# Kernel optimization log

Hardware: AMD Instinct MI355X
Metric: run time of the kernel (lower is better)

## Reference

```python
import jax, jax.numpy as jnp
import numpy as np

TOP_K = 2

def setup_inputs() -> dict:
    key = jax.random.key(0)
    k0, k1, k2, k3, k4 = jax.random.split(key, 5)
    B, S, D, H, E = 2, 2048, 1024, 2048, 8
    x = jax.random.normal(k0, (B, S, D), dtype=jnp.float32)
    router_w = jax.random.normal(k1, (D, E), dtype=jnp.float32) * (1.0 / np.sqrt(D))
    wg = jax.random.normal(k2, (E, D, H), dtype=jnp.float32) * (1.0 / np.sqrt(D))
    wu = jax.random.normal(k3, (E, D, H), dtype=jnp.float32) * (1.0 / np.sqrt(D))
    wd = jax.random.normal(k4, (E, H, D), dtype=jnp.float32) * (1.0 / np.sqrt(H))
    return {"x": x, "router_w": router_w, "wg": wg, "wu": wu, "wd": wd}

def reference(x, router_w, wg, wu, wd):
    B, S, D = x.shape
    E = router_w.shape[1]
    xf = x.reshape(-1, D)                                   # [T, D]
    router_logits = xf @ router_w                           # [T, E]
    top_logits, top_idx = jax.lax.top_k(router_logits, TOP_K)
    top_w = jax.nn.softmax(top_logits, axis=-1)             # [T, k]
    # Dense combine weights: W[t, e] = routing weight if e in top-k of t, else 0.
    combine = jnp.sum(jax.nn.one_hot(top_idx, E, dtype=x.dtype) * top_w[..., None], axis=1)  # [T, E]
    # SwiGLU experts, computed for all tokens and masked by the combine weights
    # (mathematically identical to the gather/scatter form in the original).
    gate = jnp.einsum('td,edh->eth', xf, wg)                # [E, T, H]
    up = jnp.einsum('td,edh->eth', xf, wu)                  # [E, T, H]
    fused = jax.nn.silu(gate) * up                          # [E, T, H]
    expert_out = jnp.einsum('eth,ehd->etd', fused, wd)      # [E, T, D]
    y = jnp.einsum('etd,te->td', expert_out, combine)       # [T, D]
    return y.reshape(B, S, D)
```

## Files before the change

kernel.cpp:

```cpp
#include <hip/hip_runtime.h>
#include <hip/hip_bf16.h>

#define T_TOK 4096
#define DDIM  1024
#define HDIM  2048
#define NEXP  8
#define MAXSLOT 9216

typedef __attribute__((ext_vector_type(4))) float f32x4;
typedef __attribute__((ext_vector_type(8))) short s16x8;
typedef __hip_bfloat16 bf16;

typedef const void __attribute__((address_space(1))) gvoid;
typedef void __attribute__((address_space(3))) svoid;

__device__ __forceinline__ void gload16(const void* g, void* l) {
    __builtin_amdgcn_global_load_lds((gvoid*)g, (svoid*)l, 16, 0, 0);
}

__device__ __forceinline__ int frag_off(int rr, int kq) {
    int lr = rr >> 1;
    int ch = ((rr & 1) << 2) + (kq >> 3);
    return lr * 64 + (ch ^ (lr & 7)) * 8;
}

__global__ void router_cast_kernel(const float* __restrict__ x, const float* __restrict__ rw,
                                   int* __restrict__ r_e, float* __restrict__ r_w,
                                   bf16* __restrict__ xb) {
    int wave = threadIdx.x >> 6, lane = threadIdx.x & 63;
    int t = blockIdx.x * 4 + wave;
    const float* xr = x + (size_t)t * DDIM;
    bf16* xbr = xb + (size_t)t * DDIM;
    double acc[NEXP];
#pragma unroll
    for (int e = 0; e < NEXP; ++e) acc[e] = 0.0;
#pragma unroll
    for (int c = 0; c < 4; ++c) {
        int d = c * 256 + lane * 4;
        float4 v = *reinterpret_cast<const float4*>(xr + d);
        union { ushort4 u; bf16 h[4]; } o;
        o.h[0] = __float2bfloat16(v.x);
        o.h[1] = __float2bfloat16(v.y);
        o.h[2] = __float2bfloat16(v.z);
        o.h[3] = __float2bfloat16(v.w);
        *reinterpret_cast<ushort4*>(xbr + d) = o.u;
        const float* rw0 = rw + (size_t)d * NEXP;
#pragma unroll
        for (int j = 0; j < 4; ++j) {
            float xv = (&v.x)[j];
            const float* rwr = rw0 + j * NEXP;
#pragma unroll
            for (int e = 0; e < NEXP; ++e) acc[e] += (double)xv * (double)rwr[e];
        }
    }
#pragma unroll
    for (int e = 0; e < NEXP; ++e) {
#pragma unroll
        for (int off = 32; off > 0; off >>= 1) acc[e] += __shfl_down(acc[e], off);
    }
    if (lane == 0) {
        int i0 = 0; double v0 = acc[0];
#pragma unroll
        for (int e = 1; e < NEXP; ++e) if (acc[e] > v0) { v0 = acc[e]; i0 = e; }
        int i1 = -1; double v1 = -1e300;
#pragma unroll
        for (int e = 0; e < NEXP; ++e) { if (e == i0) continue; if (acc[e] > v1) { v1 = acc[e]; i1 = e; } }
        float w0 = 1.0f / (1.0f + expf((float)(v1 - v0)));
        float w1 = 1.0f - w0;
        r_e[2*t]   = i0; r_e[2*t+1] = i1;
        r_w[2*t]   = w0; r_w[2*t+1] = w1;
    }
}

__global__ void binning_kernel(const int* __restrict__ r_e, const float* __restrict__ r_w,
                               int* __restrict__ offs, int* __restrict__ cnt,
                               int* __restrict__ list, float* __restrict__ slot_w) {
    __shared__ int scnt[NEXP], scur[NEXP], soff[NEXP + 1];
    int tid = threadIdx.x;
    if (tid < NEXP) { scnt[tid] = 0; scur[tid] = 0; }
    __syncthreads();
    for (int i = tid; i < 2 * T_TOK; i += 512) atomicAdd(&scnt[r_e[i]], 1);
    __syncthreads();
    if (tid == 0) {
        int s = 0;
        for (int e = 0; e < NEXP; ++e) { soff[e] = s; s += (scnt[e] + 127) & ~127; }
        soff[NEXP] = s;
    }
    __syncthreads();
    if (tid < NEXP + 1) offs[tid] = soff[tid];
    if (tid < NEXP) cnt[tid] = scnt[tid];
    for (int i = tid; i < 2 * T_TOK; i += 512) {
        int e = r_e[i];
        int pos = atomicAdd(&scur[e], 1);
        int slot = soff[e] + pos;
        list[slot] = i >> 1;
        slot_w[slot] = r_w[i];
    }
}

__global__ void transpose_cast_kernel(const float* __restrict__ in, bf16* __restrict__ out,
                                      int R, int C, int rmul, int roff, size_t outE) {
    __shared__ bf16 tile[64][68];
    const float* inp = in + (size_t)blockIdx.z * R * C;
    bf16* outp = out + (size_t)blockIdx.z * outE;
    int r0 = blockIdx.x * 64, c0 = blockIdx.y * 64;
    int tid = threadIdx.x;
#pragma unroll
    for (int i = 0; i < 4; ++i) {
        int idx = i * 256 + tid;
        int r = idx >> 4, c4 = (idx & 15) * 4;
        float4 v = *reinterpret_cast<const float4*>(inp + (size_t)(r0 + r) * C + c0 + c4);
        union { ushort4 u; bf16 h[4]; } o;
        o.h[0] = __float2bfloat16(v.x);
        o.h[1] = __float2bfloat16(v.y);
        o.h[2] = __float2bfloat16(v.z);
        o.h[3] = __float2bfloat16(v.w);
        *reinterpret_cast<ushort4*>(&tile[r][c4]) = o.u;
    }
    __syncthreads();
#pragma unroll
    for (int i = 0; i < 4; ++i) {
        int idx = i * 256 + tid;
        int c = idx >> 4, r4 = (idx & 15) * 4;
        union { ushort4 u; bf16 h[4]; } w;
        w.h[0] = tile[r4 + 0][c];
        w.h[1] = tile[r4 + 1][c];
        w.h[2] = tile[r4 + 2][c];
        w.h[3] = tile[r4 + 3][c];
        *reinterpret_cast<ushort4*>(outp + ((size_t)(c0 + c) * rmul + roff) * R + r0 + r4) = w.u;
    }
}

__device__ __forceinline__ int find_expert(const int* offs, int slot0) {
    int e = 0;
#pragma unroll
    for (int i = 0; i < NEXP - 1; ++i) e += (offs[e + 1] <= slot0) ? 1 : 0;
    return e;
}

__global__ __launch_bounds__(256, 2)
void gateup_kernel(const bf16* __restrict__ xb, const bf16* __restrict__ wguT,
                   const int* __restrict__ offs, const int* __restrict__ cnt,
                   const int* __restrict__ list, bf16* __restrict__ hbuf) {
    int slot0 = blockIdx.y * 128;
    if (slot0 >= offs[NEXP]) return;
    int e = find_expert(offs, slot0);
    int base = offs[e];
    int ne = cnt[e];
    int m0 = slot0 - base;
    int n0 = blockIdx.x * 128;

    __shared__ bf16 As[2][4096];
    __shared__ bf16 Bs[2][4096];

    int tid = threadIdx.x, lane = tid & 63, wid = tid >> 6;

    const bf16* bbase = wguT + (size_t)e * (2 * HDIM) * DDIM + (size_t)n0 * DDIM;

    const bf16* aS[2]; const bf16* bS[2];
    int sdst[2];
#pragma unroll
    for (int j = 0; j < 2; ++j) {
        int q = wid + j * 4;
        int lr = q * 8 + (lane >> 3);
        int ch = (lane & 7) ^ (lr & 7);
        int rr = 2 * lr + (ch >> 2);
        int koff = (ch & 3) * 8;
        int r = m0 + rr; if (r > ne - 1) r = ne - 1;
        aS[j] = xb + (size_t)list[base + r] * DDIM + koff;
        bS[j] = bbase + (size_t)rr * DDIM + koff;
        sdst[j] = q * 512;
    }

    int rl = lane & 15, kq = 8 * (lane >> 4);
    int wrow = (wid >> 1) * 64;
    int wcol = (wid & 1) * 64;
    int offA[4], offB[4];
#pragma unroll
    for (int mi = 0; mi < 4; ++mi) offA[mi] = frag_off(wrow + mi * 16 + rl, kq);
#pragma unroll
    for (int ni = 0; ni < 4; ++ni) offB[ni] = frag_off(wcol + ni * 16 + rl, kq);

    f32x4 zero4 = {0.f, 0.f, 0.f, 0.f};
    f32x4 acc[4][4];
#pragma unroll
    for (int mi = 0; mi < 4; ++mi)
#pragma unroll
        for (int ni = 0; ni < 4; ++ni) acc[mi][ni] = zero4;

    const int nk = DDIM / 32;

#define GU_STAGE(tt, buf)                                     \
    {                                                         \
        int k0 = (tt) * 32;                                   \
        gload16(aS[0] + k0, &As[buf][sdst[0]]);               \
        gload16(aS[1] + k0, &As[buf][sdst[1]]);               \
        gload16(bS[0] + k0, &Bs[buf][sdst[0]]);               \
        gload16(bS[1] + k0, &Bs[buf][sdst[1]]);               \
    }

    GU_STAGE(0, 0);
    asm volatile("s_waitcnt vmcnt(0)" ::: "memory");
    __builtin_amdgcn_s_barrier();

    int cur = 0;
    for (int t = 0; t < nk; ++t) {
        if (t + 1 < nk) GU_STAGE(t + 1, cur ^ 1);
        const bf16* Ab = As[cur];
        const bf16* Bb = Bs[cur];
        s16x8 a[4], b[4];
#pragma unroll
        for (int mi = 0; mi < 4; ++mi) a[mi] = *reinterpret_cast<const s16x8*>(Ab + offA[mi]);
#pragma unroll
        for (int ni = 0; ni < 4; ++ni) b[ni] = *reinterpret_cast<const s16x8*>(Bb + offB[ni]);
        __builtin_amdgcn_s_setprio(1);
#pragma unroll
        for (int mi = 0; mi < 4; ++mi)
#pragma unroll
            for (int ni = 0; ni < 4; ++ni)
                acc[mi][ni] = __builtin_amdgcn_mfma_f32_16x16x32_bf16(a[mi], b[ni], acc[mi][ni], 0, 0, 0);
        __builtin_amdgcn_s_setprio(0);
        __builtin_amdgcn_sched_barrier(0);
        if (t + 1 < nk) {
            asm volatile("s_waitcnt vmcnt(0)" ::: "memory");
            __builtin_amdgcn_s_barrier();
        }
        cur ^= 1;
    }
#undef GU_STAGE

    int rbase = (lane >> 4) * 4, cbase = lane & 15;
    bool evenlane = (lane & 1) == 0;
#pragma unroll
    for (int mi = 0; mi < 4; ++mi) {
#pragma unroll
        for (int ni = 0; ni < 4; ++ni) {
#pragma unroll
            for (int r = 0; r < 4; ++r) {
                float own = acc[mi][ni][r];
                float oth = __shfl_xor(own, 1);
                int row = m0 + wrow + mi * 16 + rbase + r;
                if (evenlane && row < ne) {
                    float g = own, u = oth;
                    float h = (g / (1.0f + expf(-g))) * u;
                    int hcol = (n0 + wcol + ni * 16 + cbase) >> 1;
                    hbuf[(size_t)(base + row) * HDIM + hcol] = __float2bfloat16(h);
                }
            }
        }
    }
}

__global__ __launch_bounds__(256, 2)
void down_kernel(const bf16* __restrict__ hbuf, const bf16* __restrict__ wdT,
                 const int* __restrict__ offs, const int* __restrict__ cnt,
                 const int* __restrict__ list, const float* __restrict__ slot_w,
                 float* __restrict__ y) {
    int slot0 = blockIdx.y * 128;
    if (slot0 >= offs[NEXP]) return;
    int e = find_expert(offs, slot0);
    int base = offs[e];
    int ne = cnt[e];
    int m0 = slot0 - base;
    int n0 = blockIdx.x * 128;

    __shared__ bf16 As[2][4096];
    __shared__ bf16 Bs[2][4096];

    int tid = threadIdx.x, lane = tid & 63, wid = tid >> 6;

    const bf16* bbase = wdT + (size_t)e * DDIM * HDIM + (size_t)n0 * HDIM;

    const bf16* aS[2]; const bf16* bS[2];
    int sdst[2];
#pragma unroll
    for (int j = 0; j < 2; ++j) {
        int q = wid + j * 4;
        int lr = q * 8 + (lane >> 3);
        int ch = (lane & 7) ^ (lr & 7);
        int rr = 2 * lr + (ch >> 2);
        int koff = (ch & 3) * 8;
        int r = m0 + rr; if (r > ne - 1) r = ne - 1;
        aS[j] = hbuf + (size_t)(base + r) * HDIM + koff;
        bS[j] = bbase + (size_t)rr * HDIM + koff;
        sdst[j] = q * 512;
    }

    int rl = lane & 15, kq = 8 * (lane >> 4);
    int wrow = (wid >> 1) * 64;
    int wcol = (wid & 1) * 64;
    int offA[4], offB[4];
#pragma unroll
    for (int mi = 0; mi < 4; ++mi) offA[mi] = frag_off(wrow + mi * 16 + rl, kq);
#pragma unroll
    for (int ni = 0; ni < 4; ++ni) offB[ni] = frag_off(wcol + ni * 16 + rl, kq);

    f32x4 zero4 = {0.f, 0.f, 0.f, 0.f};
    f32x4 acc[4][4];
#pragma unroll
    for (int mi = 0; mi < 4; ++mi)
#pragma unroll
        for (int ni = 0; ni < 4; ++ni) acc[mi][ni] = zero4;

    const int nk = HDIM / 32;

#define DN_STAGE(tt, buf)                                     \
    {                                                         \
        int k0 = (tt) * 32;                                   \
        gload16(aS[0] + k0, &As[buf][sdst[0]]);               \
        gload16(aS[1] + k0, &As[buf][sdst[1]]);               \
        gload16(bS[0] + k0, &Bs[buf][sdst[0]]);               \
        gload16(bS[1] + k0, &Bs[buf][sdst[1]]);               \
    }

    DN_STAGE(0, 0);
    asm volatile("s_waitcnt vmcnt(0)" ::: "memory");
    __builtin_amdgcn_s_barrier();

    int cur = 0;
    for (int t = 0; t < nk; ++t) {
        if (t + 1 < nk) DN_STAGE(t + 1, cur ^ 1);
        const bf16* Ab = As[cur];
        const bf16* Bb = Bs[cur];
        s16x8 a[4], b[4];
#pragma unroll
        for (int mi = 0; mi < 4; ++mi) a[mi] = *reinterpret_cast<const s16x8*>(Ab + offA[mi]);
#pragma unroll
        for (int ni = 0; ni < 4; ++ni) b[ni] = *reinterpret_cast<const s16x8*>(Bb + offB[ni]);
        __builtin_amdgcn_s_setprio(1);
#pragma unroll
        for (int mi = 0; mi < 4; ++mi)
#pragma unroll
            for (int ni = 0; ni < 4; ++ni)
                acc[mi][ni] = __builtin_amdgcn_mfma_f32_16x16x32_bf16(a[mi], b[ni], acc[mi][ni], 0, 0, 0);
        __builtin_amdgcn_s_setprio(0);
        __builtin_amdgcn_sched_barrier(0);
        if (t + 1 < nk) {
            asm volatile("s_waitcnt vmcnt(0)" ::: "memory");
            __builtin_amdgcn_s_barrier();
        }
        cur ^= 1;
    }
#undef DN_STAGE

    int rbase = (lane >> 4) * 4, cbase = lane & 15;
#pragma unroll
    for (int mi = 0; mi < 4; ++mi) {
#pragma unroll
        for (int r = 0; r < 4; ++r) {
            int row = m0 + wrow + mi * 16 + rbase + r;
            if (row < ne) {
                int slot = base + row;
                int tok = list[slot];
                float w = slot_w[slot];
                float* yrow = y + (size_t)tok * DDIM + n0 + wcol + cbase;
#pragma unroll
                for (int ni = 0; ni < 4; ++ni)
                    atomicAdd(yrow + ni * 16, w * acc[mi][ni][r]);
            }
        }
    }
}

extern "C" void kernel_launch(void* const* d_in, const int* in_sizes, int n_in,
                              void* d_out, int out_size, void* d_ws, size_t ws_size,
                              hipStream_t stream) {
    const float* x  = (const float*)d_in[0];
    const float* rw = (const float*)d_in[1];
    const float* wg = (const float*)d_in[2];
    const float* wu = (const float*)d_in[3];
    const float* wd = (const float*)d_in[4];
    float* y = (float*)d_out;

    char* ws = (char*)d_ws;
    int*   r_e    = (int*)  (ws + 0);
    float* r_w    = (float*)(ws + 32768);
    int*   offs   = (int*)  (ws + 65600);
    int*   cnt    = (int*)  (ws + 65544 + 96);
    int*   list   = (int*)  (ws + 65664 + 128);
    float* slot_w = (float*)(ws + 65664 + 128 + 4 * MAXSLOT);
    bf16*  xb     = (bf16*) (ws + 1048576ull);
    bf16*  wguT   = (bf16*) (ws + 16777216ull);
    bf16*  wdT    = (bf16*) (ws + 83886080ull);
    bf16*  hbuf   = (bf16*) (ws + 117440512ull);

    transpose_cast_kernel<<<dim3(DDIM / 64, HDIM / 64, NEXP), 256, 0, stream>>>(
        wg, wguT, DDIM, HDIM, 2, 0, (size_t)2 * HDIM * DDIM);
    transpose_cast_kernel<<<dim3(DDIM / 64, HDIM / 64, NEXP), 256, 0, stream>>>(
        wu, wguT, DDIM, HDIM, 2, 1, (size_t)2 * HDIM * DDIM);
    transpose_cast_kernel<<<dim3(HDIM / 64, DDIM / 64, NEXP), 256, 0, stream>>>(
        wd, wdT, HDIM, DDIM, 1, 0, (size_t)DDIM * HDIM);

    router_cast_kernel<<<dim3(T_TOK / 4), 256, 0, stream>>>(x, rw, r_e, r_w, xb);
    binning_kernel<<<dim3(1), 512, 0, stream>>>(r_e, r_w, offs, cnt, list, slot_w);

    hipMemsetAsync(d_out, 0, (size_t)out_size * sizeof(float), stream);

    gateup_kernel<<<dim3(2 * HDIM / 128, MAXSLOT / 128, 1), 256, 0, stream>>>(
        xb, wguT, offs, cnt, list, hbuf);
    down_kernel<<<dim3(DDIM / 128, MAXSLOT / 128, 1), 256, 0, stream>>>(
        hbuf, wdT, offs, cnt, list, slot_w, y);
}
```

Baseline: 289.0 us.

## Triple-buffer GEMM K-loop prefetch and merge gate/up weight transposes

```diff
diff --git a/kernel.cpp b/kernel.cpp
--- a/kernel.cpp
+++ b/kernel.cpp
@@ -98,18 +98,20 @@
     }
 }
 
-__global__ void transpose_cast_kernel(const float* __restrict__ in, bf16* __restrict__ out,
-                                      int R, int C, int rmul, int roff, size_t outE) {
+__global__ void transpose_gu_kernel(const float* __restrict__ wg, const float* __restrict__ wu,
+                                    bf16* __restrict__ wguT) {
     __shared__ bf16 tile[64][68];
-    const float* inp = in + (size_t)blockIdx.z * R * C;
-    bf16* outp = out + (size_t)blockIdx.z * outE;
+    int which = blockIdx.z >> 3;
+    int e = blockIdx.z & 7;
+    const float* inp = (which ? wu : wg) + (size_t)e * DDIM * HDIM;
+    bf16* outp = wguT + (size_t)e * 2 * HDIM * DDIM;
     int r0 = blockIdx.x * 64, c0 = blockIdx.y * 64;
     int tid = threadIdx.x;
 #pragma unroll
     for (int i = 0; i < 4; ++i) {
         int idx = i * 256 + tid;
         int r = idx >> 4, c4 = (idx & 15) * 4;
-        float4 v = *reinterpret_cast<const float4*>(inp + (size_t)(r0 + r) * C + c0 + c4);
+        float4 v = *reinterpret_cast<const float4*>(inp + (size_t)(r0 + r) * HDIM + c0 + c4);
         union { ushort4 u; bf16 h[4]; } o;
         o.h[0] = __float2bfloat16(v.x);
         o.h[1] = __float2bfloat16(v.y);
@@ -127,7 +129,39 @@
         w.h[1] = tile[r4 + 1][c];
         w.h[2] = tile[r4 + 2][c];
         w.h[3] = tile[r4 + 3][c];
-        *reinterpret_cast<ushort4*>(outp + ((size_t)(c0 + c) * rmul + roff) * R + r0 + r4) = w.u;
+        *reinterpret_cast<ushort4*>(outp + ((size_t)(c0 + c) * 2 + which) * DDIM + r0 + r4) = w.u;
+    }
+}
+
+__global__ void transpose_wd_kernel(const float* __restrict__ wd, bf16* __restrict__ wdT) {
+    __shared__ bf16 tile[64][68];
+    const float* inp = wd + (size_t)blockIdx.z * HDIM * DDIM;
+    bf16* outp = wdT + (size_t)blockIdx.z * DDIM * HDIM;
+    int r0 = blockIdx.x * 64, c0 = blockIdx.y * 64;
+    int tid = threadIdx.x;
+#pragma unroll
+    for (int i = 0; i < 4; ++i) {
+        int idx = i * 256 + tid;
+        int r = idx >> 4, c4 = (idx & 15) * 4;
+        float4 v = *reinterpret_cast<const float4*>(inp + (size_t)(r0 + r) * DDIM + c0 + c4);
+        union { ushort4 u; bf16 h[4]; } o;
+        o.h[0] = __float2bfloat16(v.x);
+        o.h[1] = __float2bfloat16(v.y);
+        o.h[2] = __float2bfloat16(v.z);
+        o.h[3] = __float2bfloat16(v.w);
+        *reinterpret_cast<ushort4*>(&tile[r][c4]) = o.u;
+    }
+    __syncthreads();
+#pragma unroll
+    for (int i = 0; i < 4; ++i) {
+        int idx = i * 256 + tid;
+        int c = idx >> 4, r4 = (idx & 15) * 4;
+        union { ushort4 u; bf16 h[4]; } w;
+        w.h[0] = tile[r4 + 0][c];
+        w.h[1] = tile[r4 + 1][c];
+        w.h[2] = tile[r4 + 2][c];
+        w.h[3] = tile[r4 + 3][c];
+        *reinterpret_cast<ushort4*>(outp + (size_t)(c0 + c) * HDIM + r0 + r4) = w.u;
     }
 }
 
@@ -150,8 +184,8 @@
     int m0 = slot0 - base;
     int n0 = blockIdx.x * 128;
 
-    __shared__ bf16 As[2][4096];
-    __shared__ bf16 Bs[2][4096];
+    __shared__ bf16 As[3][4096];
+    __shared__ bf16 Bs[3][4096];
 
     int tid = threadIdx.x, lane = tid & 63, wid = tid >> 6;
 
@@ -200,14 +234,16 @@
     }
 
     GU_STAGE(0, 0);
-    asm volatile("s_waitcnt vmcnt(0)" ::: "memory");
+    GU_STAGE(1, 1);
+    asm volatile("s_waitcnt vmcnt(4)" ::: "memory");
     __builtin_amdgcn_s_barrier();
 
-    int cur = 0;
+    int cb = 0;
     for (int t = 0; t < nk; ++t) {
-        if (t + 1 < nk) GU_STAGE(t + 1, cur ^ 1);
-        const bf16* Ab = As[cur];
-        const bf16* Bb = Bs[cur];
+        int sb = cb + 2; if (sb >= 3) sb -= 3;
+        if (t + 2 < nk) GU_STAGE(t + 2, sb);
+        const bf16* Ab = As[cb];
+        const bf16* Bb = Bs[cb];
         s16x8 a[4], b[4];
 #pragma unroll
         for (int mi = 0; mi < 4; ++mi) a[mi] = *reinterpret_cast<const s16x8*>(Ab + offA[mi]);
@@ -222,10 +258,11 @@
         __builtin_amdgcn_s_setprio(0);
         __builtin_amdgcn_sched_barrier(0);
         if (t + 1 < nk) {
-            asm volatile("s_waitcnt vmcnt(0)" ::: "memory");
+            if (t + 2 < nk) asm volatile("s_waitcnt vmcnt(4)" ::: "memory");
+            else            asm volatile("s_waitcnt vmcnt(0)" ::: "memory");
             __builtin_amdgcn_s_barrier();
         }
-        cur ^= 1;
+        cb = cb + 1; if (cb >= 3) cb -= 3;
     }
 #undef GU_STAGE
 
@@ -264,8 +301,8 @@
     int m0 = slot0 - base;
     int n0 = blockIdx.x * 128;
 
-    __shared__ bf16 As[2][4096];
-    __shared__ bf16 Bs[2][4096];
+    __shared__ bf16 As[3][4096];
+    __shared__ bf16 Bs[3][4096];
 
     int tid = threadIdx.x, lane = tid & 63, wid = tid >> 6;
 
@@ -314,14 +351,16 @@
     }
 
     DN_STAGE(0, 0);
-    asm volatile("s_waitcnt vmcnt(0)" ::: "memory");
+    DN_STAGE(1, 1);
+    asm volatile("s_waitcnt vmcnt(4)" ::: "memory");
     __builtin_amdgcn_s_barrier();
 
-    int cur = 0;
+    int cb = 0;
     for (int t = 0; t < nk; ++t) {
-        if (t + 1 < nk) DN_STAGE(t + 1, cur ^ 1);
-        const bf16* Ab = As[cur];
-        const bf16* Bb = Bs[cur];
+        int sb = cb + 2; if (sb >= 3) sb -= 3;
+        if (t + 2 < nk) DN_STAGE(t + 2, sb);
+        const bf16* Ab = As[cb];
+        const bf16* Bb = Bs[cb];
         s16x8 a[4], b[4];
 #pragma unroll
         for (int mi = 0; mi < 4; ++mi) a[mi] = *reinterpret_cast<const s16x8*>(Ab + offA[mi]);
@@ -336,10 +375,11 @@
         __builtin_amdgcn_s_setprio(0);
         __builtin_amdgcn_sched_barrier(0);
         if (t + 1 < nk) {
-            asm volatile("s_waitcnt vmcnt(0)" ::: "memory");
+            if (t + 2 < nk) asm volatile("s_waitcnt vmcnt(4)" ::: "memory");
+            else            asm volatile("s_waitcnt vmcnt(0)" ::: "memory");
             __builtin_amdgcn_s_barrier();
         }
-        cur ^= 1;
+        cb = cb + 1; if (cb >= 3) cb -= 3;
     }
 #undef DN_STAGE
 
@@ -376,20 +416,16 @@
     int*   r_e    = (int*)  (ws + 0);
     float* r_w    = (float*)(ws + 32768);
     int*   offs   = (int*)  (ws + 65600);
-    int*   cnt    = (int*)  (ws + 65544 + 96);
-    int*   list   = (int*)  (ws + 65664 + 128);
-    float* slot_w = (float*)(ws + 65664 + 128 + 4 * MAXSLOT);
+    int*   cnt    = (int*)  (ws + 65640);
+    int*   list   = (int*)  (ws + 65792);
+    float* slot_w = (float*)(ws + 65792 + 4 * MAXSLOT);
     bf16*  xb     = (bf16*) (ws + 1048576ull);
     bf16*  wguT   = (bf16*) (ws + 16777216ull);
     bf16*  wdT    = (bf16*) (ws + 83886080ull);
     bf16*  hbuf   = (bf16*) (ws + 117440512ull);
 
-    transpose_cast_kernel<<<dim3(DDIM / 64, HDIM / 64, NEXP), 256, 0, stream>>>(
-        wg, wguT, DDIM, HDIM, 2, 0, (size_t)2 * HDIM * DDIM);
-    transpose_cast_kernel<<<dim3(DDIM / 64, HDIM / 64, NEXP), 256, 0, stream>>>(
-        wu, wguT, DDIM, HDIM, 2, 1, (size_t)2 * HDIM * DDIM);
-    transpose_cast_kernel<<<dim3(HDIM / 64, DDIM / 64, NEXP), 256, 0, stream>>>(
-        wd, wdT, HDIM, DDIM, 1, 0, (size_t)DDIM * HDIM);
+    transpose_gu_kernel<<<dim3(DDIM / 64, HDIM / 64, 2 * NEXP), 256, 0, stream>>>(wg, wu, wguT);
+    transpose_wd_kernel<<<dim3(HDIM / 64, DDIM / 64, NEXP), 256, 0, stream>>>(wd, wdT);
 
     router_cast_kernel<<<dim3(T_TOK / 4), 256, 0, stream>>>(x, rw, r_e, r_w, xb);
     binning_kernel<<<dim3(1), 512, 0, stream>>>(r_e, r_w, offs, cnt, list, slot_w);
```

Result: no change. 286.2 us (-1.0%).
